# Performance work log

Hardware: AMD Instinct MI355X
Metric: run time of the kernel (lower is better)

## Reference

```python
import jax, jax.numpy as jnp
import numpy as np

B = 16384      # batch_size
G = 8          # max_groups (groups per batch element in this setup)
P = G * (G - 1) // 2   # 28 docking pairs
D = 128        # node_dim
DG = 128       # global_dim
N = B * G      # num_nodes


def setup_inputs() -> dict:
    key = jax.random.key(0)
    ks = jax.random.split(key, 10)
    node_features = jax.random.normal(ks[0], (N, D), dtype=jnp.float32)
    global_features = jax.random.normal(ks[1], (B, DG), dtype=jnp.float32)
    # every node is a group; exactly G groups per batch element, sorted batch ids
    group_mask = jnp.ones((N,), dtype=bool)
    batch = jnp.repeat(jnp.arange(B, dtype=jnp.int32), G)
    docking_valid_mask = jax.random.bernoulli(ks[2], 0.8, (B, P))
    # pair_scorer: Linear(384,128) -> ReLU -> Linear(128,64) -> ReLU -> Linear(64,1)
    W1 = jax.random.normal(ks[3], (2 * D + DG, 128), dtype=jnp.float32) * 0.05
    b1 = jax.random.normal(ks[4], (128,), dtype=jnp.float32) * 0.05
    W2 = jax.random.normal(ks[5], (128, 64), dtype=jnp.float32) * 0.05
    b2 = jax.random.normal(ks[6], (64,), dtype=jnp.float32) * 0.05
    W3 = jax.random.normal(ks[7], (64, 1), dtype=jnp.float32) * 0.05
    b3 = jax.random.normal(ks[8], (1,), dtype=jnp.float32) * 0.05
    return {
        "node_features": node_features,
        "global_features": global_features,
        "group_mask": group_mask,
        "docking_valid_mask": docking_valid_mask,
        "batch": batch,
        "W1": W1, "b1": b1, "W2": W2, "b2": b2, "W3": W3, "b3": b3,
    }


def reference(node_features, global_features, group_mask, docking_valid_mask,
              batch, W1, b1, W2, b2, W3, b3):
    # Setup guarantees group_mask is all-True and `batch` is sorted with exactly
    # G groups per batch element, so the per-batch group gathering in the original
    # nested loop reduces to a reshape. Pair enumeration order (i outer, j inner)
    # matches np.triu_indices row-major order.
    Bsz, Dg = global_features.shape
    groups = node_features.reshape(Bsz, G, -1)          # [B, G, D]
    iu, ju = np.triu_indices(G, k=1)                    # P pairs, loop order
    gi = groups[:, iu]                                  # [B, P, D]
    gj = groups[:, ju]                                  # [B, P, D]
    gf = jnp.broadcast_to(global_features[:, None, :], (Bsz, P, Dg))
    x = jnp.concatenate([gi, gj, gf], axis=-1)          # [B, P, 2D+DG]
    h = jax.nn.relu(x @ W1 + b1)
    h = jax.nn.relu(h @ W2 + b2)
    scores = (h @ W3 + b3)[..., 0]                      # [B, P]
    NEG = jnp.float32(-1e9)
    return jnp.where(docking_valid_mask, scores, NEG)
```

## Files before the change

kernel.cpp:

```cpp
#include <hip/hip_runtime.h>

typedef float    v4f    __attribute__((ext_vector_type(4)));
typedef __fp16   f16x8  __attribute__((ext_vector_type(8)));
typedef __fp16   f16x2  __attribute__((ext_vector_type(2)));
typedef short    bf16x8 __attribute__((ext_vector_type(8)));
typedef unsigned u32x4  __attribute__((ext_vector_type(4)));
typedef unsigned short u16;

__constant__ unsigned char c_pair[28] = {
  1,2,3,4,5,6,7, 10,11,12,13,14,15, 19,20,21,22,23, 28,29,30,31, 37,38,39, 46,47, 55
};

static __device__ __forceinline__ unsigned asu(float f){ union{float f;unsigned u;}v; v.f=f; return v.u; }
static __device__ __forceinline__ float lo2f(unsigned d){ union{unsigned u;float f;}v; v.u = d<<16; return v.f; }
static __device__ __forceinline__ float hi2f(unsigned d){ union{unsigned u;float f;}v; v.u = d & 0xffff0000u; return v.f; }
static __device__ __forceinline__ unsigned pkt(float lo, float hi){
  return __builtin_amdgcn_perm(asu(hi), asu(lo), 0x07060302u);
}
static __device__ __forceinline__ unsigned pkh(float lo, float hi){
  union { f16x2 h; unsigned u; } v;
  v.h = __builtin_amdgcn_cvt_pkrtz(lo, hi);
  return v.u;
}

#define WS_W1AB 0
#define WS_W1G  65536
#define WS_W2   98304
#define WS_GP   114688
#define WS_NEED 4308992

__global__ __launch_bounds__(1024)
void prep_weights(const float* __restrict__ W1, const float* __restrict__ W2, char* __restrict__ ws)
{
  const int idx = blockIdx.x * 1024 + threadIdx.x;
  if (idx < 16384) {
    const int c = idx >> 6, kp = idx & 63;
    const int part = c >> 7, cc = c & 127;
    const float a  = W1[(size_t)(part * 128 + 2 * kp) * 128 + cc];
    const float b_ = W1[(size_t)(part * 128 + 2 * kp + 1) * 128 + cc];
    *(unsigned*)(ws + WS_W1AB + (size_t)c * 256 + ((kp * 4) ^ ((c & 7) << 4))) = pkh(a, b_);
  } else if (idx < 24576) {
    const int j = idx - 16384, c = j >> 6, kp = j & 63;
    const float a  = W1[(size_t)(256 + 2 * kp) * 128 + c];
    const float b_ = W1[(size_t)(256 + 2 * kp + 1) * 128 + c];
    *(unsigned*)(ws + WS_W1G + (size_t)c * 256 + ((kp * 4) ^ ((c & 7) << 4))) = pkh(a, b_);
  } else if (idx < 28672) {
    const int j = idx - 24576, c = j >> 6, kp = j & 63;
    const float a  = W2[(size_t)(2 * kp) * 64 + c];
    const float b_ = W2[(size_t)(2 * kp + 1) * 64 + c];
    *(unsigned*)(ws + WS_W2 + (size_t)c * 256 + ((kp * 4) ^ ((c & 7) << 4))) = pkh(a, b_);
  }
}

__global__ __launch_bounds__(256)
void prep_gp(const float* __restrict__ glob, const float* __restrict__ b1, char* __restrict__ ws)
{
  __shared__ __align__(16) char sm[65536];
  const int tid = threadIdx.x;
  const int bb0 = blockIdx.x * 128;
  for (int i = tid; i < 2048; i += 256) {
    const u32x4 v = *(const u32x4*)(ws + WS_W1G + i * 16);
    *(u32x4*)(sm + 32768 + i * 16) = v;
  }
  for (int i = tid; i < 4096; i += 256) {
    const int r = i >> 5, q = i & 31;
    const float4 f = *(const float4*)(glob + (size_t)(bb0 + r) * 128 + q * 4);
    int2 w; w.x = (int)pkh(f.x, f.y); w.y = (int)pkh(f.z, f.w);
    *(int2*)(sm + r * 256 + ((q * 8) ^ ((r & 7) << 4))) = w;
  }
  __syncthreads();
  const int wave = tid >> 6, lane = tid & 63, lrow = lane & 15, lko = (lane >> 4) * 8;
  float b1c[8];
#pragma unroll
  for (int nt = 0; nt < 8; ++nt) b1c[nt] = b1[nt * 16 + lrow];
  const v4f vzero = {0.f, 0.f, 0.f, 0.f};
  v4f acc[2][8];
#pragma unroll
  for (int mt = 0; mt < 2; ++mt)
#pragma unroll
    for (int nt = 0; nt < 8; ++nt) acc[mt][nt] = vzero;
#pragma unroll
  for (int ks = 0; ks < 4; ++ks) {
    const int kb = (ks * 32 + lko) * 2;
    f16x8 af[2];
#pragma unroll
    for (int mt = 0; mt < 2; ++mt) {
      const int r = wave * 32 + mt * 16 + lrow;
      af[mt] = *(const f16x8*)(sm + r * 256 + (kb ^ ((r & 7) << 4)));
    }
#pragma unroll
    for (int nt = 0; nt < 8; ++nt) {
      const int c = nt * 16 + lrow;
      const f16x8 bfr = *(const f16x8*)(sm + 32768 + c * 256 + (kb ^ ((c & 7) << 4)));
#pragma unroll
      for (int mt = 0; mt < 2; ++mt)
        acc[mt][nt] = __builtin_amdgcn_mfma_f32_16x16x32_f16(af[mt], bfr, acc[mt][nt], 0, 0, 0);
    }
  }
#pragma unroll
  for (int mt = 0; mt < 2; ++mt)
#pragma unroll
    for (int nt = 0; nt < 8; ++nt) {
      const int c = nt * 16 + lrow;
#pragma unroll
      for (int rg = 0; rg < 4; ++rg) {
        const int m = wave * 32 + mt * 16 + (lane >> 4) * 4 + rg;
        const int batch = bb0 + m;
        const int g = batch >> 4, q = m & 15;
        *(u16*)(ws + WS_GP + (size_t)g * 4096 + q * 256 + ((c * 2) ^ ((q & 7) << 4))) =
            (u16)pkh(acc[mt][nt][rg] + b1c[nt], 0.0f);
      }
    }
}

#define M3_PA   0
#define M3_PB   16384
#define M3_ND   32768
#define M3_GP   49152
#define M3_V    53248
#define M3_SMEM 53760

__global__ __launch_bounds__(512)
void docking_main(const float* __restrict__ node, const int* __restrict__ dmask,
                  const float* __restrict__ b2, const float* __restrict__ W3,
                  const float* __restrict__ b3,
                  const char* __restrict__ ws, float* __restrict__ outp)
{
  __shared__ __align__(16) char smem[M3_SMEM];
  const int tid = threadIdx.x;
  const int wave = tid >> 6, lane = tid & 63, lrow = lane & 15, lko = (lane >> 4) * 8;
  const int wm = wave >> 2, wn = wave & 3;
  const int bb0 = blockIdx.x * 8;
  const float bias3 = *b3;
  const v4f vzero = {0.f, 0.f, 0.f, 0.f};

  for (int idx = tid; idx < 64 * 32; idx += 512) {
    const int r = idx >> 5, q = idx & 31;
    const float4 f = *(const float4*)(node + ((size_t)bb0 * 8 + r) * 128 + q * 4);
    int2 w; w.x = (int)pkh(f.x, f.y); w.y = (int)pkh(f.z, f.w);
    *(int2*)(smem + M3_ND + r * 256 + ((q * 8) ^ ((r & 7) << 4))) = w;
  }
  {
    const int q = tid >> 6, cp = tid & 63;
    const int qq = (bb0 & 15) + q;
    union { unsigned u; f16x2 h; } cv;
    cv.u = *(const unsigned*)(ws + WS_GP + ((size_t)(bb0 >> 4)) * 4096
                              + qq * 256 + ((cp * 4) ^ ((qq & 7) << 4)));
    float* gq = (float*)(smem + M3_GP) + q * 128;
    gq[cp * 2] = (float)cv.h[0]; gq[cp * 2 + 1] = (float)cv.h[1];
  }
  if (tid < 64)       ((float*)(smem + M3_V))[tid] = b2[tid];
  else if (tid < 128) ((float*)(smem + M3_V))[tid] = W3[tid - 64];
  __syncthreads();

  const char* wsW = ws + WS_W1AB;
  const int pbase = (wn >= 2) ? M3_PB : M3_PA;
  const int rgb = (lane >> 4) * 4;
  const float* sgp = (const float*)(smem + M3_GP);

  v4f acc[2][4];
#pragma unroll
  for (int mt = 0; mt < 2; ++mt)
#pragma unroll
    for (int nt = 0; nt < 4; ++nt) acc[mt][nt] = vzero;

#pragma unroll
  for (int ks = 0; ks < 4; ++ks) {
    const int kb = (ks * 32 + lko) * 2;
    f16x8 Bf[4];
#pragma unroll
    for (int nt = 0; nt < 4; ++nt) {
      const int c = wn * 64 + nt * 16 + lrow;
      Bf[nt] = *(const f16x8*)(wsW + c * 256 + (kb ^ ((c & 7) << 4)));
    }
#pragma unroll
    for (int mt = 0; mt < 2; ++mt) {
      const int rr = wm * 32 + mt * 16 + lrow;
      const f16x8 Af = *(const f16x8*)(smem + M3_ND + rr * 256 + (kb ^ ((rr & 7) << 4)));
#pragma unroll
      for (int nt = 0; nt < 4; ++nt)
        acc[mt][nt] = __builtin_amdgcn_mfma_f32_16x16x32_f16(Af, Bf[nt], acc[mt][nt], 0, 0, 0);
    }
  }
#pragma unroll
  for (int mt = 0; mt < 2; ++mt)
#pragma unroll
    for (int nt = 0; nt < 4; ++nt) {
      const int c = (wn & 1) * 64 + nt * 16 + lrow;
#pragma unroll
      for (int rg = 0; rg < 4; ++rg) {
        const int m = wm * 32 + mt * 16 + rgb + rg;
        float v = acc[mt][nt][rg];
        if (wn >= 2) v += sgp[(m >> 3) * 128 + c];
        *(u16*)(smem + pbase + m * 256 + ((c * 2) ^ ((m & 7) << 4))) =
            (u16)pkh(v, 0.0f);
      }
    }
  __syncthreads();

#pragma unroll
  for (int i = 0; i < 2; ++i) {
    const int j = tid + i * 512;
    const u32x4 v = *(const u32x4*)(ws + WS_W2 + j * 16);
    *(u32x4*)(smem + M3_ND + j * 16) = v;
  }
  __syncthreads();

  const float* sV = (const float*)(smem + M3_V);
  for (int t = wave; t < 14; t += 8) {
    const int r  = t * 16 + lrow;
    const int bb = (r * 9363) >> 18;
    const int p  = r - bb * 28;
    const unsigned pr8 = c_pair[p];
    const int mi = bb * 8 + (int)(pr8 >> 3);
    const int mj = bb * 8 + (int)(pr8 & 7);

    v4f acc2[4] = {vzero, vzero, vzero, vzero};
#pragma unroll
    for (int ks = 0; ks < 4; ++ks) {
      const int kb = (ks * 32 + lko) * 2;
      const f16x8 va = *(const f16x8*)(smem + M3_PA + mi * 256 + (kb ^ ((mi & 7) << 4)));
      const f16x8 vb = *(const f16x8*)(smem + M3_PB + mj * 256 + (kb ^ ((mj & 7) << 4)));
      f16x8 h1 = va + vb;
      h1 = __builtin_elementwise_max(h1, (f16x8)(__fp16)0.0f);
#pragma unroll
      for (int nt = 0; nt < 4; ++nt) {
        const int cc = nt * 16 + lrow;
        const f16x8 w2fr = *(const f16x8*)(smem + M3_ND + cc * 256 + (kb ^ ((cc & 7) << 4)));
        acc2[nt] = __builtin_amdgcn_mfma_f32_16x16x32_f16(h1, w2fr, acc2[nt], 0, 0, 0);
      }
    }
    float part[4] = {0.f, 0.f, 0.f, 0.f};
#pragma unroll
    for (int nt = 0; nt < 4; ++nt) {
      const int n = nt * 16 + lrow;
      const float b2v = sV[n], w3v = sV[64 + n];
#pragma unroll
      for (int rg = 0; rg < 4; ++rg)
        part[rg] += fmaxf(acc2[nt][rg] + b2v, 0.0f) * w3v;
    }
#pragma unroll
    for (int mk = 1; mk < 16; mk <<= 1)
#pragma unroll
      for (int rg = 0; rg < 4; ++rg) part[rg] += __shfl_xor(part[rg], mk, 16);

    if ((lane & 15) == 0) {
      const int rb = t * 16 + (lane >> 4) * 4;
#pragma unroll
      for (int rg = 0; rg < 4; ++rg) {
        const int rr = rb + rg;
        const int b2_ = (rr * 9363) >> 18;
        const int p2  = rr - b2_ * 28;
        const size_t o = (size_t)(bb0 + b2_) * 28 + p2;
        outp[o] = dmask[o] ? (part[rg] + bias3) : -1.0e9f;
      }
    }
  }
}

#define F_THREADS 512
#define F_NB      8
#define F_OFF_A    0
#define F_OFF_GL   16384
#define F_OFF_SB   20480
#define F_OFF_W2   53248
#define F_OFF_B1V  69632
#define F_OFF_B2V  70144
#define F_OFF_W3V  70400
#define F_SMEM     70656

__global__ __launch_bounds__(F_THREADS, 4)
void docking_fused(const float* __restrict__ node, const float* __restrict__ glob,
                   const int* __restrict__ dmask,
                   const float* __restrict__ W1, const float* __restrict__ b1,
                   const float* __restrict__ W2, const float* __restrict__ b2,
                   const float* __restrict__ W3, const float* __restrict__ b3,
                   float* __restrict__ outp)
{
  __shared__ __align__(16) char smem[F_SMEM];
  const int tid = threadIdx.x;
  const int bb0 = blockIdx.x * F_NB;
  const size_t nrow0 = (size_t)bb0 * 8;
  const float bias3 = *b3;

  if (tid < 128)      ((float*)(smem + F_OFF_B1V))[tid]       = b1[tid];
  else if (tid < 192) ((float*)(smem + F_OFF_B2V))[tid - 128] = b2[tid - 128];
  else if (tid < 256) ((float*)(smem + F_OFF_W3V))[tid - 192] = W3[tid - 192];

  for (int idx = tid; idx < 64 * 32; idx += F_THREADS) {
    const int r = idx >> 5, q = idx & 31;
    const float4 f = *(const float4*)(node + (nrow0 + (size_t)r) * 128 + q * 4);
    int2 w; w.x = (int)pkt(f.x, f.y); w.y = (int)pkt(f.z, f.w);
    *(int2*)(smem + F_OFF_A + r * 256 + ((q * 8) ^ ((r & 7) << 4))) = w;
  }
  for (int idx = tid; idx < 16 * 32; idx += F_THREADS) {
    const int r = idx >> 5, q = idx & 31;
    float4 f = make_float4(0.f, 0.f, 0.f, 0.f);
    if (r < F_NB) f = *(const float4*)(glob + (size_t)(bb0 + r) * 128 + q * 4);
    int2 w; w.x = (int)pkt(f.x, f.y); w.y = (int)pkt(f.z, f.w);
    *(int2*)(smem + F_OFF_GL + r * 256 + ((q * 8) ^ ((r & 7) << 4))) = w;
  }
  for (int idx = tid; idx < 4096; idx += F_THREADS) {
    const int cl = idx & 7, kl = (idx >> 3) & 7, ch = (idx >> 6) & 7, kh = idx >> 9;
    const int c = cl | (ch << 3), kp = kl | (kh << 3);
    const float a  = W2[(size_t)(2 * kp) * 64 + c];
    const float b_ = W2[(size_t)(2 * kp + 1) * 64 + c];
    *(unsigned*)(smem + F_OFF_W2 + c * 256 + ((kp * 4) ^ ((c & 7) << 4))) = pkt(a, b_);
  }
  auto stageB = [&](int rowOff) {
    for (int idx = tid; idx < 8192; idx += F_THREADS) {
      const int cl = idx & 7, kl = (idx >> 3) & 7, ch = (idx >> 6) & 15, kh = idx >> 10;
      const int c = cl | (ch << 3), kp = kl | (kh << 3);
      const float a  = W1[(size_t)(rowOff + 2 * kp) * 128 + c];
      const float b_ = W1[(size_t)(rowOff + 2 * kp + 1) * 128 + c];
      *(unsigned*)(smem + F_OFF_SB + c * 256 + ((kp * 4) ^ ((c & 7) << 4))) = pkt(a, b_);
    }
  };
  stageB(0);
  __syncthreads();

  const int wave = tid >> 6, lane = tid & 63;
  const int lrow = lane & 15;
  const int lko  = (lane >> 4) * 8;
  const int wmt = wave >> 1, wnh = wave & 1;
  const v4f vzero = {0.f, 0.f, 0.f, 0.f};

  bf16x8 af[4];
#pragma unroll
  for (int ks = 0; ks < 4; ++ks) {
    const int r = wmt * 16 + lrow;
    af[ks] = *(const bf16x8*)(smem + F_OFF_A + r * 256 + (((ks * 32 + lko) * 2) ^ ((r & 7) << 4)));
  }
  v4f acc_a[4] = {vzero, vzero, vzero, vzero};
#pragma unroll
  for (int ks = 0; ks < 4; ++ks) {
    const int kb = (ks * 32 + lko) * 2;
#pragma unroll
    for (int nt = 0; nt < 4; ++nt) {
      const int c = wnh * 64 + nt * 16 + lrow;
      const bf16x8 bfr = *(const bf16x8*)(smem + F_OFF_SB + c * 256 + (kb ^ ((c & 7) << 4)));
      acc_a[nt] = __builtin_amdgcn_mfma_f32_16x16x32_bf16(af[ks], bfr, acc_a[nt], 0, 0, 0);
    }
  }
  __syncthreads();
  stageB(128);
  __syncthreads();
  v4f acc_b[4] = {vzero, vzero, vzero, vzero};
#pragma unroll
  for (int ks = 0; ks < 4; ++ks) {
    const int kb = (ks * 32 + lko) * 2;
#pragma unroll
    for (int nt = 0; nt < 4; ++nt) {
      const int c = wnh * 64 + nt * 16 + lrow;
      const bf16x8 bfr = *(const bf16x8*)(smem + F_OFF_SB + c * 256 + (kb ^ ((c & 7) << 4)));
      acc_b[nt] = __builtin_amdgcn_mfma_f32_16x16x32_bf16(af[ks], bfr, acc_b[nt], 0, 0, 0);
    }
  }
  __syncthreads();
  stageB(256);
  __syncthreads();
  v4f accg = vzero;
#pragma unroll
  for (int ks = 0; ks < 4; ++ks) {
    const int kb = (ks * 32 + lko) * 2;
    const bf16x8 ag = *(const bf16x8*)(smem + F_OFF_GL + lrow * 256 + (kb ^ ((lrow & 7) << 4)));
    const int cg = wave * 16 + lrow;
    const bf16x8 bg = *(const bf16x8*)(smem + F_OFF_SB + cg * 256 + (kb ^ ((cg & 7) << 4)));
    accg = __builtin_amdgcn_mfma_f32_16x16x32_bf16(ag, bg, accg, 0, 0, 0);
  }
  __syncthreads();
  {
    const int rgb = (lane >> 4) * 4;
#pragma unroll
    for (int nt = 0; nt < 4; ++nt) {
      const int c = wnh * 64 + nt * 16 + lrow;
#pragma unroll
      for (int rg = 0; rg < 4; ++rg) {
        const int m = wmt * 16 + rgb + rg;
        const int sw = (c * 2) ^ ((m & 7) << 4);
        *(u16*)(smem + F_OFF_SB + m * 256 + sw)        = (u16)(asu(acc_a[nt][rg]) >> 16);
        *(u16*)(smem + F_OFF_SB + (64 + m) * 256 + sw) = (u16)(asu(acc_b[nt][rg]) >> 16);
      }
    }
    const int cg = wave * 16 + lrow;
    const float b1c = ((const float*)(smem + F_OFF_B1V))[cg];
#pragma unroll
    for (int rg = 0; rg < 4; ++rg) {
      const int bbr = rgb + rg;
      if (bbr < F_NB)
        *(u16*)(smem + F_OFF_A + bbr * 256 + ((cg * 2) ^ ((bbr & 7) << 4))) =
            (u16)(asu(accg[rg] + b1c) >> 16);
    }
  }
  __syncthreads();

  float b2n[4], w3n[4];
#pragma unroll
  for (int nt = 0; nt < 4; ++nt) {
    const int n = nt * 16 + lrow;
    b2n[nt] = ((const float*)(smem + F_OFF_B2V))[n];
    w3n[nt] = ((const float*)(smem + F_OFF_W3V))[n];
  }
  for (int t = wave; t < 14; t += 8) {
    const int r  = t * 16 + lrow;
    const int bb = (r * 9363) >> 18;
    const int p  = r - bb * 28;
    const unsigned pr8 = c_pair[p];
    const int mi = bb * 8 + (int)(pr8 >> 3);
    const int mj = 64 + bb * 8 + (int)(pr8 & 7);
    v4f acc2[4] = {vzero, vzero, vzero, vzero};
#pragma unroll
    for (int ks = 0; ks < 4; ++ks) {
      const int kb = (ks * 32 + lko) * 2;
      const u32x4 va = *(const u32x4*)(smem + F_OFF_SB + mi * 256 + (kb ^ ((mi & 7) << 4)));
      const u32x4 vb = *(const u32x4*)(smem + F_OFF_SB + mj * 256 + (kb ^ ((mj & 7) << 4)));
      const u32x4 vg = *(const u32x4*)(smem + F_OFF_A  + bb * 256 + (kb ^ ((bb & 7) << 4)));
      u32x4 a2;
#pragma unroll
      for (int w = 0; w < 4; ++w) {
        const float lo = fmaxf(lo2f(va[w]) + lo2f(vb[w]) + lo2f(vg[w]), 0.0f);
        const float hi = fmaxf(hi2f(va[w]) + hi2f(vb[w]) + hi2f(vg[w]), 0.0f);
        a2[w] = pkt(lo, hi);
      }
      union { u32x4 u; bf16x8 h; } cv; cv.u = a2;
#pragma unroll
      for (int nt = 0; nt < 4; ++nt) {
        const int c = nt * 16 + lrow;
        const bf16x8 w2fr = *(const bf16x8*)(smem + F_OFF_W2 + c * 256 + (kb ^ ((c & 7) << 4)));
        acc2[nt] = __builtin_amdgcn_mfma_f32_16x16x32_bf16(cv.h, w2fr, acc2[nt], 0, 0, 0);
      }
    }
    float part[4] = {0.f, 0.f, 0.f, 0.f};
#pragma unroll
    for (int nt = 0; nt < 4; ++nt)
#pragma unroll
      for (int rg = 0; rg < 4; ++rg)
        part[rg] += fmaxf(acc2[nt][rg] + b2n[nt], 0.0f) * w3n[nt];
#pragma unroll
    for (int mk = 1; mk < 16; mk <<= 1)
#pragma unroll
      for (int rg = 0; rg < 4; ++rg) part[rg] += __shfl_xor(part[rg], mk, 16);
    if ((lane & 15) == 0) {
      const int rb = t * 16 + (lane >> 4) * 4;
#pragma unroll
      for (int rg = 0; rg < 4; ++rg) {
        const int rr = rb + rg;
        const int b2_ = (rr * 9363) >> 18;
        const int p2  = rr - b2_ * 28;
        const size_t o = (size_t)(bb0 + b2_) * 28 + p2;
        outp[o] = dmask[o] ? (part[rg] + bias3) : -1.0e9f;
      }
    }
  }
}

extern "C" void kernel_launch(void* const* d_in, const int* in_sizes, int n_in,
                              void* d_out, int out_size, void* d_ws, size_t ws_size,
                              hipStream_t stream) {
  (void)in_sizes; (void)n_in; (void)out_size;
  const float* node = (const float*)d_in[0];
  const float* glob = (const float*)d_in[1];
  const int* dmsk   = (const int*)d_in[3];
  const float* W1 = (const float*)d_in[5];
  const float* b1 = (const float*)d_in[6];
  const float* W2 = (const float*)d_in[7];
  const float* b2 = (const float*)d_in[8];
  const float* W3 = (const float*)d_in[9];
  const float* b3 = (const float*)d_in[10];
  float* outp = (float*)d_out;

  if (ws_size >= (size_t)WS_NEED) {
    char* ws = (char*)d_ws;
    prep_weights<<<28, 1024, 0, stream>>>(W1, W2, ws);
    prep_gp<<<128, 256, 0, stream>>>(glob, b1, ws);
    docking_main<<<2048, 512, 0, stream>>>(node, dmsk, b2, W3, b3, ws, outp);
  } else {
    docking_fused<<<16384 / F_NB, F_THREADS, 0, stream>>>(node, glob, dmsk, W1, b1, W2, b2, W3, b3, outp);
  }
}
```

Before: 64.36 us.

## Make docking_main persistent with register prefetch of next node tile

The main kernel becomes persistent: 768 blocks loop over the 2048 tiles, and each block prefetches the next tile's node features into registers while it computes the layer-2 MFMA stage of the current tile. The first GEMM swaps its MFMA operands so each lane holds four consecutive columns, which lets the epilogue do one float4 load of global-projection data and one packed 8-byte LDS store in place of four 2-byte stores. This is meant to hide global load latency and cut per-block launch and setup costs. In exchange it uses more registers and adds extra barriers per tile iteration, which could lower occupancy.

Measured after the change: 67.23 us. 1.04x slower.

```diff
diff --git a/kernel.cpp b/kernel.cpp
--- a/kernel.cpp
+++ b/kernel.cpp
@@ -119,6 +119,8 @@
 #define M3_GP   49152
 #define M3_V    53248
 #define M3_SMEM 53760
+#define NTILES  2048
+#define PBLK    768
 
 __global__ __launch_bounds__(512)
 void docking_main(const float* __restrict__ node, const int* __restrict__ dmask,
@@ -130,131 +132,153 @@
   const int tid = threadIdx.x;
   const int wave = tid >> 6, lane = tid & 63, lrow = lane & 15, lko = (lane >> 4) * 8;
   const int wm = wave >> 2, wn = wave & 3;
-  const int bb0 = blockIdx.x * 8;
   const float bias3 = *b3;
   const v4f vzero = {0.f, 0.f, 0.f, 0.f};
-
-  for (int idx = tid; idx < 64 * 32; idx += 512) {
-    const int r = idx >> 5, q = idx & 31;
-    const float4 f = *(const float4*)(node + ((size_t)bb0 * 8 + r) * 128 + q * 4);
-    int2 w; w.x = (int)pkh(f.x, f.y); w.y = (int)pkh(f.z, f.w);
-    *(int2*)(smem + M3_ND + r * 256 + ((q * 8) ^ ((r & 7) << 4))) = w;
-  }
-  {
-    const int q = tid >> 6, cp = tid & 63;
-    const int qq = (bb0 & 15) + q;
-    union { unsigned u; f16x2 h; } cv;
-    cv.u = *(const unsigned*)(ws + WS_GP + ((size_t)(bb0 >> 4)) * 4096
-                              + qq * 256 + ((cp * 4) ^ ((qq & 7) << 4)));
-    float* gq = (float*)(smem + M3_GP) + q * 128;
-    gq[cp * 2] = (float)cv.h[0]; gq[cp * 2 + 1] = (float)cv.h[1];
-  }
+  const char* wsW = ws + WS_W1AB;
+  const int pbase = (wn >= 2) ? M3_PB : M3_PA;
+
   if (tid < 64)       ((float*)(smem + M3_V))[tid] = b2[tid];
   else if (tid < 128) ((float*)(smem + M3_V))[tid] = W3[tid - 64];
-  __syncthreads();
-
-  const char* wsW = ws + WS_W1AB;
-  const int pbase = (wn >= 2) ? M3_PB : M3_PA;
-  const int rgb = (lane >> 4) * 4;
-  const float* sgp = (const float*)(smem + M3_GP);
-
-  v4f acc[2][4];
-#pragma unroll
-  for (int mt = 0; mt < 2; ++mt)
-#pragma unroll
-    for (int nt = 0; nt < 4; ++nt) acc[mt][nt] = vzero;
-
-#pragma unroll
-  for (int ks = 0; ks < 4; ++ks) {
-    const int kb = (ks * 32 + lko) * 2;
-    f16x8 Bf[4];
-#pragma unroll
-    for (int nt = 0; nt < 4; ++nt) {
-      const int c = wn * 64 + nt * 16 + lrow;
-      Bf[nt] = *(const f16x8*)(wsW + c * 256 + (kb ^ ((c & 7) << 4)));
-    }
-#pragma unroll
-    for (int mt = 0; mt < 2; ++mt) {
-      const int rr = wm * 32 + mt * 16 + lrow;
-      const f16x8 Af = *(const f16x8*)(smem + M3_ND + rr * 256 + (kb ^ ((rr & 7) << 4)));
-#pragma unroll
-      for (int nt = 0; nt < 4; ++nt)
-        acc[mt][nt] = __builtin_amdgcn_mfma_f32_16x16x32_f16(Af, Bf[nt], acc[mt][nt], 0, 0, 0);
-    }
-  }
-#pragma unroll
-  for (int mt = 0; mt < 2; ++mt)
-#pragma unroll
-    for (int nt = 0; nt < 4; ++nt) {
-      const int c = (wn & 1) * 64 + nt * 16 + lrow;
-#pragma unroll
-      for (int rg = 0; rg < 4; ++rg) {
-        const int m = wm * 32 + mt * 16 + rgb + rg;
-        float v = acc[mt][nt][rg];
-        if (wn >= 2) v += sgp[(m >> 3) * 128 + c];
-        *(u16*)(smem + pbase + m * 256 + ((c * 2) ^ ((m & 7) << 4))) =
-            (u16)pkh(v, 0.0f);
-      }
-    }
-  __syncthreads();
-
-#pragma unroll
-  for (int i = 0; i < 2; ++i) {
-    const int j = tid + i * 512;
-    const u32x4 v = *(const u32x4*)(ws + WS_W2 + j * 16);
-    *(u32x4*)(smem + M3_ND + j * 16) = v;
-  }
-  __syncthreads();
-
-  const float* sV = (const float*)(smem + M3_V);
-  for (int t = wave; t < 14; t += 8) {
-    const int r  = t * 16 + lrow;
-    const int bb = (r * 9363) >> 18;
-    const int p  = r - bb * 28;
-    const unsigned pr8 = c_pair[p];
-    const int mi = bb * 8 + (int)(pr8 >> 3);
-    const int mj = bb * 8 + (int)(pr8 & 7);
-
-    v4f acc2[4] = {vzero, vzero, vzero, vzero};
+
+  auto loadND = [&](int tile, float4* pf) {
+#pragma unroll
+    for (int i = 0; i < 4; ++i) {
+      const int idx = tid + i * 512;
+      const int r = idx >> 5, q = idx & 31;
+      pf[i] = *(const float4*)(node + ((size_t)tile * 64 + r) * 128 + q * 4);
+    }
+  };
+
+  int tile = blockIdx.x;
+  float4 pf[4];
+  loadND(tile, pf);
+
+  while (tile < NTILES) {
+    const int bb0 = tile * 8;
+#pragma unroll
+    for (int i = 0; i < 4; ++i) {
+      const int idx = tid + i * 512;
+      const int r = idx >> 5, q = idx & 31;
+      int2 w; w.x = (int)pkh(pf[i].x, pf[i].y); w.y = (int)pkh(pf[i].z, pf[i].w);
+      *(int2*)(smem + M3_ND + r * 256 + ((q * 8) ^ ((r & 7) << 4))) = w;
+    }
+    {
+      const int q = tid >> 6, cp = tid & 63;
+      const int qq = (bb0 & 15) + q;
+      union { unsigned u; f16x2 h; } cv;
+      cv.u = *(const unsigned*)(ws + WS_GP + ((size_t)(bb0 >> 4)) * 4096
+                                + qq * 256 + ((cp * 4) ^ ((qq & 7) << 4)));
+      float* gq = (float*)(smem + M3_GP) + q * 128;
+      gq[cp * 2] = (float)cv.h[0]; gq[cp * 2 + 1] = (float)cv.h[1];
+    }
+    __syncthreads();
+
+    v4f acc[2][4];
+#pragma unroll
+    for (int mt = 0; mt < 2; ++mt)
+#pragma unroll
+      for (int nt = 0; nt < 4; ++nt) acc[mt][nt] = vzero;
+
 #pragma unroll
     for (int ks = 0; ks < 4; ++ks) {
       const int kb = (ks * 32 + lko) * 2;
-      const f16x8 va = *(const f16x8*)(smem + M3_PA + mi * 256 + (kb ^ ((mi & 7) << 4)));
-      const f16x8 vb = *(const f16x8*)(smem + M3_PB + mj * 256 + (kb ^ ((mj & 7) << 4)));
-      f16x8 h1 = va + vb;
-      h1 = __builtin_elementwise_max(h1, (f16x8)(__fp16)0.0f);
+      f16x8 Bf[4];
 #pragma unroll
       for (int nt = 0; nt < 4; ++nt) {
-        const int cc = nt * 16 + lrow;
-        const f16x8 w2fr = *(const f16x8*)(smem + M3_ND + cc * 256 + (kb ^ ((cc & 7) << 4)));
-        acc2[nt] = __builtin_amdgcn_mfma_f32_16x16x32_f16(h1, w2fr, acc2[nt], 0, 0, 0);
-      }
-    }
-    float part[4] = {0.f, 0.f, 0.f, 0.f};
-#pragma unroll
-    for (int nt = 0; nt < 4; ++nt) {
-      const int n = nt * 16 + lrow;
-      const float b2v = sV[n], w3v = sV[64 + n];
-#pragma unroll
-      for (int rg = 0; rg < 4; ++rg)
-        part[rg] += fmaxf(acc2[nt][rg] + b2v, 0.0f) * w3v;
-    }
-#pragma unroll
-    for (int mk = 1; mk < 16; mk <<= 1)
-#pragma unroll
-      for (int rg = 0; rg < 4; ++rg) part[rg] += __shfl_xor(part[rg], mk, 16);
-
-    if ((lane & 15) == 0) {
-      const int rb = t * 16 + (lane >> 4) * 4;
-#pragma unroll
-      for (int rg = 0; rg < 4; ++rg) {
-        const int rr = rb + rg;
-        const int b2_ = (rr * 9363) >> 18;
-        const int p2  = rr - b2_ * 28;
-        const size_t o = (size_t)(bb0 + b2_) * 28 + p2;
-        outp[o] = dmask[o] ? (part[rg] + bias3) : -1.0e9f;
-      }
-    }
+        const int c = wn * 64 + nt * 16 + lrow;
+        Bf[nt] = *(const f16x8*)(wsW + c * 256 + (kb ^ ((c & 7) << 4)));
+      }
+#pragma unroll
+      for (int mt = 0; mt < 2; ++mt) {
+        const int rr = wm * 32 + mt * 16 + lrow;
+        const f16x8 Af = *(const f16x8*)(smem + M3_ND + rr * 256 + (kb ^ ((rr & 7) << 4)));
+#pragma unroll
+        for (int nt = 0; nt < 4; ++nt)
+          acc[mt][nt] = __builtin_amdgcn_mfma_f32_16x16x32_f16(Bf[nt], Af, acc[mt][nt], 0, 0, 0);
+      }
+    }
+#pragma unroll
+    for (int mt = 0; mt < 2; ++mt) {
+      const int m = wm * 32 + mt * 16 + lrow;
+#pragma unroll
+      for (int nt = 0; nt < 4; ++nt) {
+        const int cb = (wn & 1) * 64 + nt * 16 + (lane >> 4) * 4;
+        float v0 = acc[mt][nt][0], v1 = acc[mt][nt][1];
+        float v2 = acc[mt][nt][2], v3 = acc[mt][nt][3];
+        if (wn >= 2) {
+          const float4 g = *(const float4*)((const float*)(smem + M3_GP) + (m >> 3) * 128 + cb);
+          v0 += g.x; v1 += g.y; v2 += g.z; v3 += g.w;
+        }
+        int2 w; w.x = (int)pkh(v0, v1); w.y = (int)pkh(v2, v3);
+        *(int2*)(smem + pbase + m * 256 + ((cb * 2) ^ ((m & 7) << 4))) = w;
+      }
+    }
+    __syncthreads();
+
+#pragma unroll
+    for (int i = 0; i < 2; ++i) {
+      const int j = tid + i * 512;
+      const u32x4 v = *(const u32x4*)(ws + WS_W2 + j * 16);
+      *(u32x4*)(smem + M3_ND + j * 16) = v;
+    }
+    __syncthreads();
+
+    const int ntile = tile + PBLK;
+    if (ntile < NTILES) loadND(ntile, pf);
+
+    const float* sV = (const float*)(smem + M3_V);
+    for (int t = wave; t < 14; t += 8) {
+      const int r  = t * 16 + lrow;
+      const int bb = (r * 9363) >> 18;
+      const int p  = r - bb * 28;
+      const unsigned pr8 = c_pair[p];
+      const int mi = bb * 8 + (int)(pr8 >> 3);
+      const int mj = bb * 8 + (int)(pr8 & 7);
+
+      v4f acc2[4] = {vzero, vzero, vzero, vzero};
+#pragma unroll
+      for (int ks = 0; ks < 4; ++ks) {
+        const int kb = (ks * 32 + lko) * 2;
+        const f16x8 va = *(const f16x8*)(smem + M3_PA + mi * 256 + (kb ^ ((mi & 7) << 4)));
+        const f16x8 vb = *(const f16x8*)(smem + M3_PB + mj * 256 + (kb ^ ((mj & 7) << 4)));
+        f16x8 h1 = va + vb;
+        h1 = __builtin_elementwise_max(h1, (f16x8)(__fp16)0.0f);
+#pragma unroll
+        for (int nt = 0; nt < 4; ++nt) {
+          const int cc = nt * 16 + lrow;
+          const f16x8 w2fr = *(const f16x8*)(smem + M3_ND + cc * 256 + (kb ^ ((cc & 7) << 4)));
+          acc2[nt] = __builtin_amdgcn_mfma_f32_16x16x32_f16(h1, w2fr, acc2[nt], 0, 0, 0);
+        }
+      }
+      float part[4] = {0.f, 0.f, 0.f, 0.f};
+#pragma unroll
+      for (int nt = 0; nt < 4; ++nt) {
+        const int n = nt * 16 + lrow;
+        const float b2v = sV[n], w3v = sV[64 + n];
+#pragma unroll
+        for (int rg = 0; rg < 4; ++rg)
+          part[rg] += fmaxf(acc2[nt][rg] + b2v, 0.0f) * w3v;
+      }
+#pragma unroll
+      for (int mk = 1; mk < 16; mk <<= 1)
+#pragma unroll
+        for (int rg = 0; rg < 4; ++rg) part[rg] += __shfl_xor(part[rg], mk, 16);
+
+      if ((lane & 15) == 0) {
+        const int rb = t * 16 + (lane >> 4) * 4;
+#pragma unroll
+        for (int rg = 0; rg < 4; ++rg) {
+          const int rr = rb + rg;
+          const int b2_ = (rr * 9363) >> 18;
+          const int p2  = rr - b2_ * 28;
+          const size_t o = (size_t)(bb0 + b2_) * 28 + p2;
+          outp[o] = dmask[o] ? (part[rg] + bias3) : -1.0e9f;
+        }
+      }
+    }
+
+    tile = ntile;
+    if (tile < NTILES) __syncthreads();
   }
 }
 
@@ -473,7 +497,7 @@
     char* ws = (char*)d_ws;
     prep_weights<<<28, 1024, 0, stream>>>(W1, W2, ws);
     prep_gp<<<128, 256, 0, stream>>>(glob, b1, ws);
-    docking_main<<<2048, 512, 0, stream>>>(node, dmsk, b2, W3, b3, ws, outp);
+    docking_main<<<PBLK, 512, 0, stream>>>(node, dmsk, b2, W3, b3, ws, outp);
   } else {
     docking_fused<<<16384 / F_NB, F_THREADS, 0, stream>>>(node, glob, dmsk, W1, b1, W2, b2, W3, b3, outp);
   }
```

## Swap MFMA operands for vectorized P stores and read W2 from global

Applied to the files above, without the earlier changes.

Swaps the MFMA A/B operands in the node projection so each lane holds four consecutive output columns. The half-precision results and the global-feature bias add can then be packed into 8-byte LDS stores, replacing scalar 2-byte stores. The separate barrier and the copy of W2 into shared memory are removed, and the layer-2 MFMA reads W2 fragments straight from the global workspace through cache. The shared-memory regions are reordered so the node tile no longer shares space with W2. The trade-off is W2 loads that now hit global/L2 memory inside the pair loop instead of LDS.

Measured after the change: 63.02 us. -2.1%, faster.

```diff
diff --git a/kernel.cpp b/kernel.cpp
--- a/kernel.cpp
+++ b/kernel.cpp
@@ -113,9 +113,9 @@
     }
 }
 
-#define M3_PA   0
-#define M3_PB   16384
-#define M3_ND   32768
+#define M3_ND   0
+#define M3_PA   16384
+#define M3_PB   32768
 #define M3_GP   49152
 #define M3_V    53248
 #define M3_SMEM 53760
@@ -133,6 +133,9 @@
   const int bb0 = blockIdx.x * 8;
   const float bias3 = *b3;
   const v4f vzero = {0.f, 0.f, 0.f, 0.f};
+  const char* wsW = ws + WS_W1AB;
+  const char* wsW2 = ws + WS_W2;
+  const int pbase = (wn >= 2) ? M3_PB : M3_PA;
 
   for (int idx = tid; idx < 64 * 32; idx += 512) {
     const int r = idx >> 5, q = idx & 31;
@@ -153,11 +156,6 @@
   else if (tid < 128) ((float*)(smem + M3_V))[tid] = W3[tid - 64];
   __syncthreads();
 
-  const char* wsW = ws + WS_W1AB;
-  const int pbase = (wn >= 2) ? M3_PB : M3_PA;
-  const int rgb = (lane >> 4) * 4;
-  const float* sgp = (const float*)(smem + M3_GP);
-
   v4f acc[2][4];
 #pragma unroll
   for (int mt = 0; mt < 2; ++mt)
@@ -179,30 +177,24 @@
       const f16x8 Af = *(const f16x8*)(smem + M3_ND + rr * 256 + (kb ^ ((rr & 7) << 4)));
 #pragma unroll
       for (int nt = 0; nt < 4; ++nt)
-        acc[mt][nt] = __builtin_amdgcn_mfma_f32_16x16x32_f16(Af, Bf[nt], acc[mt][nt], 0, 0, 0);
-    }
-  }
-#pragma unroll
-  for (int mt = 0; mt < 2; ++mt)
-#pragma unroll
-    for (int nt = 0; nt < 4; ++nt) {
-      const int c = (wn & 1) * 64 + nt * 16 + lrow;
-#pragma unroll
-      for (int rg = 0; rg < 4; ++rg) {
-        const int m = wm * 32 + mt * 16 + rgb + rg;
-        float v = acc[mt][nt][rg];
-        if (wn >= 2) v += sgp[(m >> 3) * 128 + c];
-        *(u16*)(smem + pbase + m * 256 + ((c * 2) ^ ((m & 7) << 4))) =
-            (u16)pkh(v, 0.0f);
-      }
-    }
-  __syncthreads();
-
-#pragma unroll
-  for (int i = 0; i < 2; ++i) {
-    const int j = tid + i * 512;
-    const u32x4 v = *(const u32x4*)(ws + WS_W2 + j * 16);
-    *(u32x4*)(smem + M3_ND + j * 16) = v;
+        acc[mt][nt] = __builtin_amdgcn_mfma_f32_16x16x32_f16(Bf[nt], Af, acc[mt][nt], 0, 0, 0);
+    }
+  }
+#pragma unroll
+  for (int mt = 0; mt < 2; ++mt) {
+    const int m = wm * 32 + mt * 16 + lrow;
+#pragma unroll
+    for (int nt = 0; nt < 4; ++nt) {
+      const int cb = (wn & 1) * 64 + nt * 16 + (lane >> 4) * 4;
+      float v0 = acc[mt][nt][0], v1 = acc[mt][nt][1];
+      float v2 = acc[mt][nt][2], v3 = acc[mt][nt][3];
+      if (wn >= 2) {
+        const float4 g = *(const float4*)((const float*)(smem + M3_GP) + (m >> 3) * 128 + cb);
+        v0 += g.x; v1 += g.y; v2 += g.z; v3 += g.w;
+      }
+      int2 w; w.x = (int)pkh(v0, v1); w.y = (int)pkh(v2, v3);
+      *(int2*)(smem + pbase + m * 256 + ((cb * 2) ^ ((m & 7) << 4))) = w;
+    }
   }
   __syncthreads();
 
@@ -226,7 +218,7 @@
 #pragma unroll
       for (int nt = 0; nt < 4; ++nt) {
         const int cc = nt * 16 + lrow;
-        const f16x8 w2fr = *(const f16x8*)(smem + M3_ND + cc * 256 + (kb ^ ((cc & 7) << 4)));
+        const f16x8 w2fr = *(const f16x8*)(wsW2 + cc * 256 + (kb ^ ((cc & 7) << 4)));
         acc2[nt] = __builtin_amdgcn_mfma_f32_16x16x32_f16(h1, w2fr, acc2[nt], 0, 0, 0);
       }
     }
```
